# Optimization experiments

Measured on AMD Instinct MI355X. Metric: run time of the kernel, lower is better.

Reference implementation:

```python
import jax, jax.numpy as jnp
import numpy as np

B, N, C, H = 2, 4096, 512, 8
D = C // H          # head dim = 64
EPS = 1e-5          # nn.LayerNorm default eps


def _layernorm(x, gamma, beta):
    m = jnp.mean(x, axis=-1, keepdims=True)
    v = jnp.var(x, axis=-1, keepdims=True)
    return (x - m) * jax.lax.rsqrt(v + EPS) * gamma + beta


def setup_inputs() -> dict:
    key = jax.random.key(0)
    k_x, k_w = jax.random.split(key, 2)
    return {
        "x": jax.random.normal(k_x, (B, N, C), dtype=jnp.float32),
        "w_qkv": jax.random.normal(k_w, (C, 3 * C), dtype=jnp.float32) * 0.02,
        "b_qkv": jnp.zeros((3 * C,), dtype=jnp.float32),
        "g_pre": jnp.ones((C,), dtype=jnp.float32),
        "beta_pre": jnp.zeros((C,), dtype=jnp.float32),
        "g_post": jnp.ones((C,), dtype=jnp.float32),
        "beta_post": jnp.zeros((C,), dtype=jnp.float32),
    }


def reference(x, w_qkv, b_qkv, g_pre, beta_pre, g_post, beta_post):
    b, n, c = x.shape
    xn = _layernorm(x, g_pre, beta_pre)                       # pre_norm (x is reassigned in source)
    qkv = (xn @ w_qkv + b_qkv).reshape(b, n, 3, H, D)
    qkv = jnp.transpose(qkv, (2, 0, 3, 1, 4))                 # [3, B, H, N, D]
    q, k, v = qkv[0], qkv[1], qkv[2]
    scale = D ** (-0.5)
    attn = jnp.einsum('bhnd,bhmd->bhnm', q, k) * scale        # [B, H, N, N]
    soft = jax.nn.softmax(attn, axis=-1)
    val = jnp.einsum('bhnm,bhmd->bhnd', soft, v)              # [B, H, N, D]
    val = jnp.transpose(val, (0, 2, 1, 3)).reshape(b, n, c)   # [B, N, C]
    val = _layernorm(val, g_post, beta_post)                  # post_norm
    return xn + val                                            # residual uses pre-normed x (faithful)
```

## Files before the change

kernel.cpp:

```cpp
#include <hip/hip_runtime.h>

#define BB   2
#define NN   4096
#define CC   512
#define HH   8
#define DD   64
#define MR   8192
#define NC3  1536
#define PS   4194304

typedef __attribute__((ext_vector_type(8))) short short8;
typedef __attribute__((ext_vector_type(4))) float floatx4;

__device__ inline unsigned short f2bf(float f) {
  unsigned int u = __float_as_uint(f);
  u = (u + 0x7fffu + ((u >> 16) & 1u)) >> 16;
  return (unsigned short)u;
}

__device__ inline unsigned int pack_bf2(float a, float b) {
  unsigned int ua = __float_as_uint(a) + 0x8000u;
  unsigned int ub = __float_as_uint(b) + 0x8000u;
  return (ub & 0xffff0000u) | (ua >> 16);
}

__device__ inline floatx4 fzero4() { floatx4 z = {0.f, 0.f, 0.f, 0.f}; return z; }

__device__ inline void async_cp16(const void* g, void* l) {
  __builtin_amdgcn_global_load_lds(
      (const __attribute__((address_space(1))) unsigned int*)g,
      (__attribute__((address_space(3))) unsigned int*)l, 16, 0, 0);
}

__global__ void convert_w_kernel(const float* __restrict__ w, unsigned short* __restrict__ wt) {
  int tid = blockIdx.x * 256 + threadIdx.x;
  int n = tid >> 9;
  int k = tid & 511;
  wt[tid] = f2bf(w[k * NC3 + n]);
}

__global__ void pre_ln_kernel(const float* __restrict__ x, const float* __restrict__ g,
                              const float* __restrict__ be, float* __restrict__ xn,
                              unsigned short* __restrict__ xnb) {
  int row = blockIdx.x;
  const float2* xr = (const float2*)(x + (size_t)row * CC);
  float2 v = xr[threadIdx.x];
  float s  = v.x + v.y;
  float sq = v.x * v.x + v.y * v.y;
  __shared__ float sm[10];
  for (int off = 32; off; off >>= 1) {
    s  += __shfl_down(s,  off, 64);
    sq += __shfl_down(sq, off, 64);
  }
  int w = threadIdx.x >> 6;
  if ((threadIdx.x & 63) == 0) { sm[w] = s; sm[4 + w] = sq; }
  __syncthreads();
  if (threadIdx.x == 0) {
    sm[8] = sm[0] + sm[1] + sm[2] + sm[3];
    sm[9] = sm[4] + sm[5] + sm[6] + sm[7];
  }
  __syncthreads();
  float mean = sm[8] * (1.0f / CC);
  float var  = sm[9] * (1.0f / CC) - mean * mean;
  float rstd = rsqrtf(var + 1e-5f);
  int i0 = threadIdx.x * 2, i1 = i0 + 1;
  float a = (v.x - mean) * rstd * g[i0] + be[i0];
  float b = (v.y - mean) * rstd * g[i1] + be[i1];
  size_t base = (size_t)row * CC;
  xn[base + i0] = a;          xn[base + i1] = b;
  xnb[base + i0] = f2bf(a);   xnb[base + i1] = f2bf(b);
}

#define QSCALE 0.180336879f

__global__ __launch_bounds__(256) void qkv_gemm_kernel(
    const unsigned short* __restrict__ xnb, const unsigned short* __restrict__ wt,
    const float* __restrict__ bias, unsigned short* __restrict__ qkvb) {
  __shared__ __align__(16) char smem[34816];
  short (*As)[64] = (short (*)[64])smem;
  short (*Bs)[64] = (short (*)[64])(smem + 16384);
  short (*T)[136] = (short (*)[136])smem;

  int tn = blockIdx.x;
  int tm = blockIdx.y;
  int tid = threadIdx.x;
  int wv = tid >> 6, lane = tid & 63;
  int quad = lane >> 4, l16 = lane & 15;
  int wm = wv >> 1, wn = wv & 1;
  int l7 = l16 & 7;

  int kr = lane >> 3;
  int kg = (lane & 7) ^ kr;

  floatx4 acc[4][4];
  for (int i = 0; i < 4; i++) for (int j = 0; j < 4; j++) acc[i][j] = fzero4();

  for (int k0 = 0; k0 < 512; k0 += 64) {
    __syncthreads();
    for (int i = 0; i < 4; i++) {
      int rowbase = i * 32 + wv * 8;
      async_cp16(&xnb[(size_t)(tm * 128 + rowbase + kr) * 512 + k0 + kg * 8], &As[rowbase][0]);
      async_cp16(&wt [(size_t)(tn * 128 + rowbase + kr) * 512 + k0 + kg * 8], &Bs[rowbase][0]);
    }
    __syncthreads();
    for (int kk = 0; kk < 2; kk++) {
      short8 a[4], b[4];
      for (int mt = 0; mt < 4; mt++)
        a[mt] = *(const short8*)&As[wm * 64 + mt * 16 + l16][((kk * 4 + quad) ^ l7) * 8];
      for (int nt = 0; nt < 4; nt++)
        b[nt] = *(const short8*)&Bs[wn * 64 + nt * 16 + l16][((kk * 4 + quad) ^ l7) * 8];
      for (int mt = 0; mt < 4; mt++)
        for (int nt = 0; nt < 4; nt++)
          acc[mt][nt] = __builtin_amdgcn_mfma_f32_16x16x32_bf16(a[mt], b[nt], acc[mt][nt], 0, 0, 0);
    }
  }
  __syncthreads();

  int part = tn >> 2;
  int b = tm >> 5;
  int tloc = (tm & 31) * 128;

  if (part < 2) {
    for (int nt = 0; nt < 4; nt++) {
      int coll = wn * 64 + nt * 16 + l16;
      float bv = bias[tn * 128 + coll];
      for (int mt = 0; mt < 4; mt++) {
        int rowb = wm * 64 + mt * 16 + quad * 4;
        for (int r = 0; r < 4; r++) {
          float v = acc[mt][nt][r] + bv;
          if (part == 0) v *= QSCALE;
          T[rowb + r][coll] = (short)f2bf(v);
        }
      }
    }
    __syncthreads();
    int h0 = (tn & 3) * 2;
    for (int it = 0; it < 8; it++) {
      int row = it * 16 + (tid >> 4);
      int l = tid & 15;
      uint4 vv = *(uint4*)&T[row][l * 8];
      int h = h0 + (l >> 3), d = (l & 7) * 8;
      size_t idx = (size_t)part * PS +
                   ((size_t)((b * 8 + h) * 4096 + tloc + row)) * 64 + d;
      *(uint4*)&qkvb[idx] = vv;
    }
  } else {
    for (int nt = 0; nt < 4; nt++) {
      int coll = wn * 64 + nt * 16 + l16;
      float bv = bias[tn * 128 + coll];
      for (int mt = 0; mt < 4; mt++) {
        int rowb = wm * 64 + mt * 16 + quad * 4;
        uint2 w;
        w.x = pack_bf2(acc[mt][nt][0] + bv, acc[mt][nt][1] + bv);
        w.y = pack_bf2(acc[mt][nt][2] + bv, acc[mt][nt][3] + bv);
        *(uint2*)&T[coll][rowb] = w;
      }
    }
    __syncthreads();
    for (int it = 0; it < 8; it++) {
      int vrow = it * 16 + (tid >> 4);
      int l = tid & 15;
      uint4 vv = *(uint4*)&T[vrow][l * 8];
      int gj = tn * 128 + vrow;
      int h = (gj >> 6) & 7, d = gj & 63;
      size_t idx = 2 * (size_t)PS +
                   ((size_t)((b * 8 + h) * 64 + d)) * 4096 + tloc + l * 8;
      *(uint4*)&qkvb[idx] = vv;
    }
  }
}

#define SMEM_ATT (16384 + 32768 + 18432)

__global__ __launch_bounds__(256, 2) void attn_kernel(
    const unsigned short* __restrict__ qkvb, float* __restrict__ val) {
  __shared__ __align__(16) char smem[SMEM_ATT];
  short (*Ks)[64]   = (short (*)[64])smem;
  short (*Vt0)[128] = (short (*)[128])(smem + 16384);
  short (*Vt1)[128] = (short (*)[128])(smem + 32768);
  short (*Psl)[72]  = (short (*)[72])(smem + 49152);
  float (*slab)[68] = (float (*)[68])smem;

  int bh = blockIdx.y;
  int qb = blockIdx.x * 128;
  int tid = threadIdx.x;
  int wv = tid >> 6, lane = tid & 63, quad = lane >> 4, l16 = lane & 15;
  int l7 = l16 & 7;
  const unsigned short* Qg = qkvb + (size_t)bh * NN * DD;
  const unsigned short* Kg = qkvb + (size_t)PS + (size_t)bh * NN * DD;
  const unsigned short* Vg = qkvb + 2 * (size_t)PS + (size_t)bh * DD * NN;

  int kr = lane >> 3;
  int kg = (lane & 7) ^ kr;
  int vr = lane >> 4;
  int vgr = (lane & 15) ^ ((wv * 4 + vr) & 15);

  for (int i = 0; i < 4; i++) {
    int rowbase = i * 32 + wv * 8;
    async_cp16(&Qg[(size_t)(qb + rowbase + kr) * 64 + kg * 8], &Ks[rowbase][0]);
  }
  __syncthreads();
  short8 qf[2][2];
  for (int g = 0; g < 2; g++)
    for (int kk = 0; kk < 2; kk++)
      qf[g][kk] = *(const short8*)&Ks[wv * 32 + g * 16 + l16][((kk * 4 + quad) ^ l7) * 8];
  __syncthreads();

  for (int i = 0; i < 4; i++) {
    int rb = i * 32 + wv * 8;
    async_cp16(&Kg[(size_t)(rb + kr) * 64 + kg * 8], &Ks[rb][0]);
  }
  for (int i = 0; i < 4; i++) {
    int rb = i * 16 + wv * 4;
    async_cp16(&Vg[(size_t)(rb + vr) * NN + vgr * 8], &Vt0[rb][0]);
  }

  floatx4 o[2][4];
  for (int g = 0; g < 2; g++) for (int dt = 0; dt < 4; dt++) o[g][dt] = fzero4();
  float ls[2] = {0.0f, 0.0f};

  short* psrow0 = &Psl[wv * 32 + l16][0];
  short* psrow1 = &Psl[wv * 32 + 16 + l16][0];

  for (int kt = 0; kt < 32; kt++) {
    __syncthreads();
    short (*Vc)[128] = (kt & 1) ? Vt1 : Vt0;
    short (*Vn)[128] = (kt & 1) ? Vt0 : Vt1;
    if (kt < 31) {
      int kn = (kt + 1) * 128;
      for (int i = 0; i < 4; i++) {
        int rb = i * 16 + wv * 4;
        async_cp16(&Vg[(size_t)(rb + vr) * NN + kn + vgr * 8], &Vn[rb][0]);
      }
    }

    floatx4 s[2][8];
    for (int nt = 0; nt < 8; nt++) {
      short8 kf0 = *(const short8*)&Ks[nt * 16 + l16][((quad) ^ l7) * 8];
      short8 kf1 = *(const short8*)&Ks[nt * 16 + l16][((4 + quad) ^ l7) * 8];
      floatx4 s0 = fzero4(), s1 = fzero4();
      s0 = __builtin_amdgcn_mfma_f32_16x16x32_bf16(kf0, qf[0][0], s0, 0, 0, 0);
      s0 = __builtin_amdgcn_mfma_f32_16x16x32_bf16(kf1, qf[0][1], s0, 0, 0, 0);
      s1 = __builtin_amdgcn_mfma_f32_16x16x32_bf16(kf0, qf[1][0], s1, 0, 0, 0);
      s1 = __builtin_amdgcn_mfma_f32_16x16x32_bf16(kf1, qf[1][1], s1, 0, 0, 0);
      s[0][nt] = s0;
      s[1][nt] = s1;
    }
    __syncthreads();
    if (kt < 31) {
      int kn = (kt + 1) * 128;
      for (int i = 0; i < 4; i++) {
        int rb = i * 32 + wv * 8;
        async_cp16(&Kg[(size_t)(kn + rb + kr) * 64 + kg * 8], &Ks[rb][0]);
      }
    }

    for (int hf = 0; hf < 2; hf++) {
      for (int n4 = 0; n4 < 4; n4++) {
        int nt = hf * 4 + n4;
        float p00 = __builtin_amdgcn_exp2f(s[0][nt][0]);
        float p01 = __builtin_amdgcn_exp2f(s[0][nt][1]);
        float p02 = __builtin_amdgcn_exp2f(s[0][nt][2]);
        float p03 = __builtin_amdgcn_exp2f(s[0][nt][3]);
        float p10 = __builtin_amdgcn_exp2f(s[1][nt][0]);
        float p11 = __builtin_amdgcn_exp2f(s[1][nt][1]);
        float p12 = __builtin_amdgcn_exp2f(s[1][nt][2]);
        float p13 = __builtin_amdgcn_exp2f(s[1][nt][3]);
        ls[0] += (p00 + p01) + (p02 + p03);
        ls[1] += (p10 + p11) + (p12 + p13);
        uint2 w0, w1;
        w0.x = pack_bf2(p00, p01);  w0.y = pack_bf2(p02, p03);
        w1.x = pack_bf2(p10, p11);  w1.y = pack_bf2(p12, p13);
        *(uint2*)&psrow0[n4 * 16 + quad * 4] = w0;
        *(uint2*)&psrow1[n4 * 16 + quad * 4] = w1;
      }
      for (int ks = 0; ks < 2; ks++) {
        int ksg = hf * 2 + ks;
        short8 pa0 = *(const short8*)&Psl[wv * 32 + l16][ks * 32 + quad * 8];
        short8 pa1 = *(const short8*)&Psl[wv * 32 + 16 + l16][ks * 32 + quad * 8];
        for (int dt = 0; dt < 4; dt++) {
          short8 vb = *(const short8*)&Vc[dt * 16 + l16][((ksg * 4 + quad) ^ l16) * 8];
          o[0][dt] = __builtin_amdgcn_mfma_f32_16x16x32_bf16(vb, pa0, o[0][dt], 0, 0, 0);
          o[1][dt] = __builtin_amdgcn_mfma_f32_16x16x32_bf16(vb, pa1, o[1][dt], 0, 0, 0);
        }
      }
    }
  }

  for (int g = 0; g < 2; g++) {
    ls[g] += __shfl_xor(ls[g], 16, 64);
    ls[g] += __shfl_xor(ls[g], 32, 64);
  }

  __syncthreads();
  for (int g = 0; g < 2; g++) {
    float inv = 1.0f / ls[g];
    int q = wv * 32 + g * 16 + l16;
    for (int dt = 0; dt < 4; dt++)
      for (int r = 0; r < 4; r++)
        slab[q][dt * 16 + quad * 4 + r] = o[g][dt][r] * inv;
  }
  __syncthreads();
  int b = bh >> 3, h = bh & 7;
  for (int it = 0; it < 8; it++) {
    int row = it * 16 + (tid >> 4);
    int col4 = (tid & 15) * 4;
    float4 vv = *(float4*)&slab[row][col4];
    *(float4*)&val[((size_t)(b * 4096 + qb + row)) * 512 + h * 64 + col4] = vv;
  }
}

__global__ void post_ln_kernel(const float* __restrict__ valp, const float* __restrict__ xn,
                               const float* __restrict__ g, const float* __restrict__ be,
                               float* __restrict__ out) {
  int row = blockIdx.x;
  const float2* vr = (const float2*)(valp + (size_t)row * CC);
  float2 v = vr[threadIdx.x];
  float s  = v.x + v.y;
  float sq = v.x * v.x + v.y * v.y;
  __shared__ float sm[10];
  for (int off = 32; off; off >>= 1) {
    s  += __shfl_down(s,  off, 64);
    sq += __shfl_down(sq, off, 64);
  }
  int w = threadIdx.x >> 6;
  if ((threadIdx.x & 63) == 0) { sm[w] = s; sm[4 + w] = sq; }
  __syncthreads();
  if (threadIdx.x == 0) {
    sm[8] = sm[0] + sm[1] + sm[2] + sm[3];
    sm[9] = sm[4] + sm[5] + sm[6] + sm[7];
  }
  __syncthreads();
  float mean = sm[8] * (1.0f / CC);
  float var  = sm[9] * (1.0f / CC) - mean * mean;
  float rstd = rsqrtf(var + 1e-5f);
  int i0 = threadIdx.x * 2, i1 = i0 + 1;
  size_t base = (size_t)row * CC;
  out[base + i0] = (v.x - mean) * rstd * g[i0] + be[i0] + xn[base + i0];
  out[base + i1] = (v.y - mean) * rstd * g[i1] + be[i1] + xn[base + i1];
}

extern "C" void kernel_launch(void* const* d_in, const int* in_sizes, int n_in,
                              void* d_out, int out_size, void* d_ws, size_t ws_size,
                              hipStream_t stream) {
  const float* x       = (const float*)d_in[0];
  const float* w_qkv   = (const float*)d_in[1];
  const float* b_qkv   = (const float*)d_in[2];
  const float* g_pre   = (const float*)d_in[3];
  const float* be_pre  = (const float*)d_in[4];
  const float* g_post  = (const float*)d_in[5];
  const float* be_post = (const float*)d_in[6];
  float* out = (float*)d_out;

  float* xn  = (float*)d_ws;
  float* val = xn + 4194304;
  unsigned short* xnb  = (unsigned short*)(val + 4194304);
  unsigned short* qkvb = xnb + 4194304;
  unsigned short* wt   = qkvb + 3 * (size_t)PS;

  convert_w_kernel<<<3072, 256, 0, stream>>>(w_qkv, wt);
  pre_ln_kernel<<<MR, 256, 0, stream>>>(x, g_pre, be_pre, xn, xnb);
  qkv_gemm_kernel<<<dim3(12, 64), 256, 0, stream>>>(xnb, wt, b_qkv, qkvb);
  attn_kernel<<<dim3(32, 16), 256, 0, stream>>>(qkvb, val);
  post_ln_kernel<<<MR, 256, 0, stream>>>(val, xn, g_post, be_post, out);
}
```

Before: 211.5 us.

## Vectorize layernorms, tile weight transpose, and double-buffer QKV GEMM loads

The weight conversion now goes through a shared-memory tile, so both its reads and its writes are coalesced and vectorized. Both layernorm kernels switch to one wave per row with float4 loads and stores and a shuffle-only reduction, which removes the shared-memory syncs. The QKV GEMM double-buffers its LDS tiles, prefetching the next K slice asynchronously while computing the current one. This doubles the GEMM's shared memory, which may lower occupancy. The bf16 packing in pre-LN now uses a round-half-up path instead of round-to-nearest-even.

```diff
diff --git a/kernel.cpp b/kernel.cpp
--- a/kernel.cpp
+++ b/kernel.cpp
@@ -32,43 +32,70 @@
       (__attribute__((address_space(3))) unsigned int*)l, 16, 0, 0);
 }
 
-__global__ void convert_w_kernel(const float* __restrict__ w, unsigned short* __restrict__ wt) {
-  int tid = blockIdx.x * 256 + threadIdx.x;
-  int n = tid >> 9;
-  int k = tid & 511;
-  wt[tid] = f2bf(w[k * NC3 + n]);
-}
-
-__global__ void pre_ln_kernel(const float* __restrict__ x, const float* __restrict__ g,
-                              const float* __restrict__ be, float* __restrict__ xn,
-                              unsigned short* __restrict__ xnb) {
-  int row = blockIdx.x;
-  const float2* xr = (const float2*)(x + (size_t)row * CC);
-  float2 v = xr[threadIdx.x];
-  float s  = v.x + v.y;
-  float sq = v.x * v.x + v.y * v.y;
-  __shared__ float sm[10];
-  for (int off = 32; off; off >>= 1) {
-    s  += __shfl_down(s,  off, 64);
-    sq += __shfl_down(sq, off, 64);
-  }
-  int w = threadIdx.x >> 6;
-  if ((threadIdx.x & 63) == 0) { sm[w] = s; sm[4 + w] = sq; }
-  __syncthreads();
-  if (threadIdx.x == 0) {
-    sm[8] = sm[0] + sm[1] + sm[2] + sm[3];
-    sm[9] = sm[4] + sm[5] + sm[6] + sm[7];
-  }
-  __syncthreads();
-  float mean = sm[8] * (1.0f / CC);
-  float var  = sm[9] * (1.0f / CC) - mean * mean;
+__global__ __launch_bounds__(256) void convert_w_kernel(
+    const float* __restrict__ w, unsigned short* __restrict__ wt) {
+  __shared__ short T[64][68];
+  int bn = blockIdx.x;
+  int bk = blockIdx.y;
+  int tid = threadIdx.x;
+  for (int p = 0; p < 4; p++) {
+    int k = p * 16 + (tid >> 4);
+    int n4 = (tid & 15) * 4;
+    float4 v = *(const float4*)&w[(size_t)(bk * 64 + k) * NC3 + bn * 64 + n4];
+    T[n4 + 0][k] = (short)f2bf(v.x);
+    T[n4 + 1][k] = (short)f2bf(v.y);
+    T[n4 + 2][k] = (short)f2bf(v.z);
+    T[n4 + 3][k] = (short)f2bf(v.w);
+  }
+  __syncthreads();
+  for (int p = 0; p < 2; p++) {
+    int n = p * 32 + (tid >> 3);
+    int k8 = (tid & 7) * 8;
+    uint4 v = *(uint4*)&T[n][k8];
+    *(uint4*)&wt[(size_t)(bn * 64 + n) * 512 + bk * 64 + k8] = v;
+  }
+}
+
+__global__ __launch_bounds__(256) void pre_ln_kernel(
+    const float* __restrict__ x, const float* __restrict__ g,
+    const float* __restrict__ be, float* __restrict__ xn,
+    unsigned short* __restrict__ xnb) {
+  int wv = threadIdx.x >> 6, lane = threadIdx.x & 63;
+  int row = blockIdx.x * 4 + wv;
+  const float4* xr = (const float4*)(x + (size_t)row * CC);
+  float4 v0 = xr[lane];
+  float4 v1 = xr[64 + lane];
+  float s  = (v0.x + v0.y) + (v0.z + v0.w) + (v1.x + v1.y) + (v1.z + v1.w);
+  float sq = (v0.x * v0.x + v0.y * v0.y) + (v0.z * v0.z + v0.w * v0.w) +
+             (v1.x * v1.x + v1.y * v1.y) + (v1.z * v1.z + v1.w * v1.w);
+  for (int off = 1; off < 64; off <<= 1) {
+    s  += __shfl_xor(s,  off, 64);
+    sq += __shfl_xor(sq, off, 64);
+  }
+  float mean = s * (1.0f / CC);
+  float var  = sq * (1.0f / CC) - mean * mean;
   float rstd = rsqrtf(var + 1e-5f);
-  int i0 = threadIdx.x * 2, i1 = i0 + 1;
-  float a = (v.x - mean) * rstd * g[i0] + be[i0];
-  float b = (v.y - mean) * rstd * g[i1] + be[i1];
+  const float4* gg = (const float4*)g;
+  const float4* bb = (const float4*)be;
+  float4 g0 = gg[lane], g1 = gg[64 + lane];
+  float4 b0 = bb[lane], b1 = bb[64 + lane];
+  float4 o0, o1;
+  o0.x = (v0.x - mean) * rstd * g0.x + b0.x;
+  o0.y = (v0.y - mean) * rstd * g0.y + b0.y;
+  o0.z = (v0.z - mean) * rstd * g0.z + b0.z;
+  o0.w = (v0.w - mean) * rstd * g0.w + b0.w;
+  o1.x = (v1.x - mean) * rstd * g1.x + b1.x;
+  o1.y = (v1.y - mean) * rstd * g1.y + b1.y;
+  o1.z = (v1.z - mean) * rstd * g1.z + b1.z;
+  o1.w = (v1.w - mean) * rstd * g1.w + b1.w;
   size_t base = (size_t)row * CC;
-  xn[base + i0] = a;          xn[base + i1] = b;
-  xnb[base + i0] = f2bf(a);   xnb[base + i1] = f2bf(b);
+  ((float4*)(xn + base))[lane] = o0;
+  ((float4*)(xn + base))[64 + lane] = o1;
+  uint2 u0, u1;
+  u0.x = pack_bf2(o0.x, o0.y); u0.y = pack_bf2(o0.z, o0.w);
+  u1.x = pack_bf2(o1.x, o1.y); u1.y = pack_bf2(o1.z, o1.w);
+  *(uint2*)&xnb[base + 4 * lane] = u0;
+  *(uint2*)&xnb[base + 256 + 4 * lane] = u1;
 }
 
 #define QSCALE 0.180336879f
@@ -76,9 +103,13 @@
 __global__ __launch_bounds__(256) void qkv_gemm_kernel(
     const unsigned short* __restrict__ xnb, const unsigned short* __restrict__ wt,
     const float* __restrict__ bias, unsigned short* __restrict__ qkvb) {
-  __shared__ __align__(16) char smem[34816];
-  short (*As)[64] = (short (*)[64])smem;
-  short (*Bs)[64] = (short (*)[64])(smem + 16384);
+  __shared__ __align__(16) char smem[65536];
+  short (*Asb[2])[64];
+  short (*Bsb[2])[64];
+  Asb[0] = (short (*)[64])smem;
+  Bsb[0] = (short (*)[64])(smem + 16384);
+  Asb[1] = (short (*)[64])(smem + 32768);
+  Bsb[1] = (short (*)[64])(smem + 49152);
   short (*T)[136] = (short (*)[136])smem;
 
   int tn = blockIdx.x;
@@ -95,14 +126,26 @@
   floatx4 acc[4][4];
   for (int i = 0; i < 4; i++) for (int j = 0; j < 4; j++) acc[i][j] = fzero4();
 
-  for (int k0 = 0; k0 < 512; k0 += 64) {
+  for (int i = 0; i < 4; i++) {
+    int rb = i * 32 + wv * 8;
+    async_cp16(&xnb[(size_t)(tm * 128 + rb + kr) * 512 + kg * 8], &Asb[0][rb][0]);
+    async_cp16(&wt [(size_t)(tn * 128 + rb + kr) * 512 + kg * 8], &Bsb[0][rb][0]);
+  }
+
+  for (int it = 0; it < 8; it++) {
     __syncthreads();
-    for (int i = 0; i < 4; i++) {
-      int rowbase = i * 32 + wv * 8;
-      async_cp16(&xnb[(size_t)(tm * 128 + rowbase + kr) * 512 + k0 + kg * 8], &As[rowbase][0]);
-      async_cp16(&wt [(size_t)(tn * 128 + rowbase + kr) * 512 + k0 + kg * 8], &Bs[rowbase][0]);
-    }
-    __syncthreads();
+    short (*As)[64] = Asb[it & 1];
+    short (*Bs)[64] = Bsb[it & 1];
+    if (it < 7) {
+      int kn = (it + 1) * 64;
+      short (*An)[64] = Asb[(it + 1) & 1];
+      short (*Bn)[64] = Bsb[(it + 1) & 1];
+      for (int i = 0; i < 4; i++) {
+        int rb = i * 32 + wv * 8;
+        async_cp16(&xnb[(size_t)(tm * 128 + rb + kr) * 512 + kn + kg * 8], &An[rb][0]);
+        async_cp16(&wt [(size_t)(tn * 128 + rb + kr) * 512 + kn + kg * 8], &Bn[rb][0]);
+      }
+    }
     for (int kk = 0; kk < 2; kk++) {
       short8 a[4], b[4];
       for (int mt = 0; mt < 4; mt++)
@@ -310,34 +353,42 @@
   }
 }
 
-__global__ void post_ln_kernel(const float* __restrict__ valp, const float* __restrict__ xn,
-                               const float* __restrict__ g, const float* __restrict__ be,
-                               float* __restrict__ out) {
-  int row = blockIdx.x;
-  const float2* vr = (const float2*)(valp + (size_t)row * CC);
-  float2 v = vr[threadIdx.x];
-  float s  = v.x + v.y;
-  float sq = v.x * v.x + v.y * v.y;
-  __shared__ float sm[10];
-  for (int off = 32; off; off >>= 1) {
-    s  += __shfl_down(s,  off, 64);
-    sq += __shfl_down(sq, off, 64);
-  }
-  int w = threadIdx.x >> 6;
-  if ((threadIdx.x & 63) == 0) { sm[w] = s; sm[4 + w] = sq; }
-  __syncthreads();
-  if (threadIdx.x == 0) {
-    sm[8] = sm[0] + sm[1] + sm[2] + sm[3];
-    sm[9] = sm[4] + sm[5] + sm[6] + sm[7];
-  }
-  __syncthreads();
-  float mean = sm[8] * (1.0f / CC);
-  float var  = sm[9] * (1.0f / CC) - mean * mean;
+__global__ __launch_bounds__(256) void post_ln_kernel(
+    const float* __restrict__ valp, const float* __restrict__ xn,
+    const float* __restrict__ g, const float* __restrict__ be,
+    float* __restrict__ out) {
+  int wv = threadIdx.x >> 6, lane = threadIdx.x & 63;
+  int row = blockIdx.x * 4 + wv;
+  const float4* vr = (const float4*)(valp + (size_t)row * CC);
+  float4 v0 = vr[lane];
+  float4 v1 = vr[64 + lane];
+  float s  = (v0.x + v0.y) + (v0.z + v0.w) + (v1.x + v1.y) + (v1.z + v1.w);
+  float sq = (v0.x * v0.x + v0.y * v0.y) + (v0.z * v0.z + v0.w * v0.w) +
+             (v1.x * v1.x + v1.y * v1.y) + (v1.z * v1.z + v1.w * v1.w);
+  for (int off = 1; off < 64; off <<= 1) {
+    s  += __shfl_xor(s,  off, 64);
+    sq += __shfl_xor(sq, off, 64);
+  }
+  float mean = s * (1.0f / CC);
+  float var  = sq * (1.0f / CC) - mean * mean;
   float rstd = rsqrtf(var + 1e-5f);
-  int i0 = threadIdx.x * 2, i1 = i0 + 1;
-  size_t base = (size_t)row * CC;
-  out[base + i0] = (v.x - mean) * rstd * g[i0] + be[i0] + xn[base + i0];
-  out[base + i1] = (v.y - mean) * rstd * g[i1] + be[i1] + xn[base + i1];
+  const float4* gg = (const float4*)g;
+  const float4* bb = (const float4*)be;
+  float4 g0 = gg[lane], g1 = gg[64 + lane];
+  float4 b0 = bb[lane], b1 = bb[64 + lane];
+  const float4* xr = (const float4*)(xn + (size_t)row * CC);
+  float4 x0 = xr[lane], x1 = xr[64 + lane];
+  float4 o0, o1;
+  o0.x = (v0.x - mean) * rstd * g0.x + b0.x + x0.x;
+  o0.y = (v0.y - mean) * rstd * g0.y + b0.y + x0.y;
+  o0.z = (v0.z - mean) * rstd * g0.z + b0.z + x0.z;
+  o0.w = (v0.w - mean) * rstd * g0.w + b0.w + x0.w;
+  o1.x = (v1.x - mean) * rstd * g1.x + b1.x + x1.x;
+  o1.y = (v1.y - mean) * rstd * g1.y + b1.y + x1.y;
+  o1.z = (v1.z - mean) * rstd * g1.z + b1.z + x1.z;
+  o1.w = (v1.w - mean) * rstd * g1.w + b1.w + x1.w;
+  ((float4*)(out + (size_t)row * CC))[lane] = o0;
+  ((float4*)(out + (size_t)row * CC))[64 + lane] = o1;
 }
 
 extern "C" void kernel_launch(void* const* d_in, const int* in_sizes, int n_in,
@@ -358,9 +409,9 @@
   unsigned short* qkvb = xnb + 4194304;
   unsigned short* wt   = qkvb + 3 * (size_t)PS;
 
-  convert_w_kernel<<<3072, 256, 0, stream>>>(w_qkv, wt);
-  pre_ln_kernel<<<MR, 256, 0, stream>>>(x, g_pre, be_pre, xn, xnb);
+  convert_w_kernel<<<dim3(24, 8), 256, 0, stream>>>(w_qkv, wt);
+  pre_ln_kernel<<<2048, 256, 0, stream>>>(x, g_pre, be_pre, xn, xnb);
   qkv_gemm_kernel<<<dim3(12, 64), 256, 0, stream>>>(xnb, wt, b_qkv, qkvb);
   attn_kernel<<<dim3(32, 16), 256, 0, stream>>>(qkvb, val);
-  post_ln_kernel<<<MR, 256, 0, stream>>>(val, xn, g_post, be_post, out);
-}
+  post_ln_kernel<<<2048, 256, 0, stream>>>(val, xn, g_post, be_post, out);
+}
```

Measured after the change: 206.3 us. 1.03x faster.
